# Kernel tuning notes

Measured on AMD Instinct MI355X. Metric: run time of the kernel, lower is better.

The kernel has to match this reference:

```python
import jax, jax.numpy as jnp
import numpy as np

B, Q, PAST = 2, 1024, 1024
T = Q + PAST
HID, NH, NKV, HD = 4096, 32, 8, 128
MAXPOS = 4096
SCALE = HD ** -0.5


def setup_inputs() -> dict:
    key = jax.random.key(0)
    ks = jax.random.split(key, 8)
    hidden_states = jax.random.normal(ks[0], (B, Q, HID), jnp.float32)
    attention_mask = jnp.ones((B, T), jnp.int32)  # all tokens valid
    position_ids = jnp.broadcast_to(
        jnp.arange(PAST, PAST + Q, dtype=jnp.int64)[None, :], (B, Q))
    # standard RoPE caches: [max_pos, head_dim/2]
    inv = 1.0 / (10000.0 ** (np.arange(0, HD, 2, dtype=np.float64) / HD))
    ang = np.arange(MAXPOS, dtype=np.float64)[:, None] * inv[None, :]
    rope_cos_freqs = jnp.asarray(np.cos(ang), jnp.float32)
    rope_sin_freqs = jnp.asarray(np.sin(ang), jnp.float32)
    past_key = jax.random.normal(ks[1], (B, NKV, PAST, HD), jnp.float32)
    past_value = jax.random.normal(ks[2], (B, NKV, PAST, HD), jnp.float32)
    q_w = jax.random.normal(ks[3], (NH * HD, HID), jnp.float32) * 0.02
    k_w = jax.random.normal(ks[4], (NKV * HD, HID), jnp.float32) * 0.02
    v_w = jax.random.normal(ks[5], (NKV * HD, HID), jnp.float32) * 0.02
    o_w = jax.random.normal(ks[6], (HID, NH * HD), jnp.float32) * 0.02
    return {"hidden_states": hidden_states, "attention_mask": attention_mask,
            "position_ids": position_ids, "rope_cos_freqs": rope_cos_freqs,
            "rope_sin_freqs": rope_sin_freqs, "past_key": past_key,
            "past_value": past_value, "q_w": q_w, "k_w": k_w, "v_w": v_w,
            "o_w": o_w}


def _rope(x, cos, sin):
    # x: [B,S,n_heads,HD]; cos/sin: [B,S,HD/2]; non-interleaved (half split)
    d2 = x.shape[-1] // 2
    x1, x2 = x[..., :d2], x[..., d2:]
    c, s = cos[:, :, None, :], sin[:, :, None, :]
    return jnp.concatenate([x1 * c - x2 * s, x2 * c + x1 * s], axis=-1)


def reference(hidden_states, attention_mask, position_ids, rope_cos_freqs,
              rope_sin_freqs, past_key, past_value, q_w, k_w, v_w, o_w):
    b, q_len, _ = hidden_states.shape
    q = jnp.einsum('bsh,oh->bso', hidden_states, q_w).reshape(b, q_len, NH, HD)
    k = jnp.einsum('bsh,oh->bso', hidden_states, k_w).reshape(b, q_len, NKV, HD)
    v = jnp.einsum('bsh,oh->bso', hidden_states, v_w).reshape(b, q_len, NKV, HD)

    cos = rope_cos_freqs[position_ids]  # [B,Q,HD/2]
    sin = rope_sin_freqs[position_ids]
    q = _rope(q, cos, sin)
    k = _rope(k, cos, sin)

    # append to KV cache -> [B,NKV,T,HD]
    present_key = jnp.concatenate([past_key, k.transpose(0, 2, 1, 3)], axis=2)
    present_value = jnp.concatenate([past_value, v.transpose(0, 2, 1, 3)], axis=2)

    # additive causal + padding mask built from cumsum of attention_mask
    all_idx = jnp.cumsum(attention_mask, axis=-1)            # [B,T]
    full = (all_idx[:, -q_len:, None] >= all_idx[:, None, :]) \
        & attention_mask[:, None, :].astype(bool)            # [B,Q,T]
    bias = jnp.where(full, 0.0, -10000.0)[:, None, :, :]     # [B,1,Q,T]

    group = NH // NKV
    k_rep = jnp.repeat(present_key, group, axis=1)           # [B,NH,T,HD]
    v_rep = jnp.repeat(present_value, group, axis=1)

    scores = jnp.einsum('bqhd,bhkd->bhqk', q, k_rep) * SCALE + bias
    probs = jax.nn.softmax(scores, axis=-1)
    ctx = jnp.einsum('bhqk,bhkd->bqhd', probs, v_rep).reshape(b, q_len, NH * HD)
    attn_out = jnp.einsum('bso,ho->bsh', ctx, o_w)
    return attn_out, present_key, present_value
```

## Files before the change

kernel.cpp:

```cpp
#include <hip/hip_runtime.h>
#include <hip/hip_bf16.h>
#include <stdint.h>

typedef __bf16 bf16_t;
typedef bf16_t bf16x8 __attribute__((ext_vector_type(8)));
typedef bf16_t bf16x4 __attribute__((ext_vector_type(4)));
typedef float f32x4 __attribute__((ext_vector_type(4)));

#define B_ 2
#define Q_ 1024
#define PAST_ 1024
#define T_ 2048
#define HID_ 4096
#define NH_ 32
#define NKV_ 8
#define HD_ 128
#define SCALE_ 0.08838834764831845f

__device__ __forceinline__ void async_cp16(const bf16_t* g, bf16_t* l) {
  __builtin_amdgcn_global_load_lds((__attribute__((address_space(1))) void*)g,
                                   (__attribute__((address_space(3))) void*)l, 16, 0, 0);
}

__global__ void cvt_f32_bf16(const float* __restrict__ src, bf16_t* __restrict__ dst, size_t n) {
  size_t i = ((size_t)blockIdx.x * blockDim.x + threadIdx.x) * 8;
  if (i >= n) return;
  float4 a = *(const float4*)(src + i);
  float4 b = *(const float4*)(src + i + 4);
  bf16x8 o;
  o[0] = (bf16_t)a.x; o[1] = (bf16_t)a.y; o[2] = (bf16_t)a.z; o[3] = (bf16_t)a.w;
  o[4] = (bf16_t)b.x; o[5] = (bf16_t)b.y; o[6] = (bf16_t)b.z; o[7] = (bf16_t)b.w;
  *(bf16x8*)(dst + i) = o;
}

__global__ void copy_past(const float* __restrict__ pk, const float* __restrict__ pv,
                          float* __restrict__ oK, float* __restrict__ oV,
                          bf16_t* __restrict__ Kall) {
  size_t i = ((size_t)blockIdx.x * 256 + threadIdx.x) * 4;
  if (i >= (size_t)B_ * NKV_ * PAST_ * HD_) return;
  int d = (int)(i & 127);
  size_t r = i >> 7;
  int t = (int)(r & 1023); r >>= 10;
  int g = (int)(r & 7); int b = (int)(r >> 3);
  size_t dst = (((size_t)b * NKV_ + g) * T_ + t) * HD_ + d;
  float4 k4 = *(const float4*)(pk + i);
  float4 v4 = *(const float4*)(pv + i);
  *(float4*)(oK + dst) = k4;
  *(float4*)(oV + dst) = v4;
  bf16x4 kb; kb[0] = (bf16_t)k4.x; kb[1] = (bf16_t)k4.y; kb[2] = (bf16_t)k4.z; kb[3] = (bf16_t)k4.w;
  *(bf16x4*)(Kall + dst) = kb;
}

__global__ void build_vt(const float* __restrict__ past_v, const float* __restrict__ QKV,
                         bf16_t* __restrict__ Vt) {
  __shared__ bf16_t tile[64][136];
  const int tid = threadIdx.x;
  const int t0 = blockIdx.x * 64, g = blockIdx.y, b = blockIdx.z;
#pragma unroll
  for (int k = 0; k < 8; ++k) {
    int idx = k * 256 + tid;
    int t = idx >> 5, dc = (idx & 31) * 4;
    int tt = t0 + t;
    const float* src = (tt < PAST_)
        ? past_v + ((((size_t)b * NKV_ + g) * PAST_ + tt) * HD_ + dc)
        : QKV + (((size_t)b * Q_ + (tt - PAST_)) * 6144 + 5120 + g * HD_ + dc);
    float4 v4 = *(const float4*)src;
    tile[t][dc] = (bf16_t)v4.x; tile[t][dc + 1] = (bf16_t)v4.y;
    tile[t][dc + 2] = (bf16_t)v4.z; tile[t][dc + 3] = (bf16_t)v4.w;
  }
  __syncthreads();
#pragma unroll
  for (int k = 0; k < 4; ++k) {
    int idx = k * 256 + tid;
    int d = idx >> 3, c = idx & 7;
    bf16x8 o;
#pragma unroll
    for (int j = 0; j < 8; ++j) o[j] = tile[c * 8 + j][d];
    *(bf16x8*)(Vt + ((((size_t)b * NKV_ + g) * HD_ + d) * T_) + t0 + c * 8) = o;
  }
}

__global__ __launch_bounds__(256)
void gemm_bt(const bf16_t* __restrict__ A, const bf16_t* __restrict__ W,
             float* __restrict__ C, int M, int N, int K) {
  __shared__ bf16_t lA[128 * 64];
  __shared__ bf16_t lB[128 * 64];
  const int tid = threadIdx.x;
  const int wave = tid >> 6, lane = tid & 63;
  const int quad = lane >> 4, l15 = lane & 15;
  const int bm = blockIdx.y * 128, bn = blockIdx.x * 128;
  const int wm = (wave >> 1) * 64, wn = (wave & 1) * 64;
  f32x4 acc[4][4] = {};
  for (int k0 = 0; k0 < K; k0 += 64) {
    __syncthreads();
#pragma unroll
    for (int t = 0; t < 4; ++t) {
      int cb = t * 256 + wave * 64;
      int c = cb + lane;
      int row = c >> 3, sc = (c & 7) ^ (row & 7);
      async_cp16(A + (size_t)(bm + row) * K + k0 + sc * 8, lA + (size_t)cb * 8);
      async_cp16(W + (size_t)(bn + row) * K + k0 + sc * 8, lB + (size_t)cb * 8);
    }
    __syncthreads();
#pragma unroll
    for (int ks = 0; ks < 2; ++ks) {
      bf16x8 af[4], bfr[4];
      int lchunk = ks * 4 + quad;
      int pc = (lchunk ^ (l15 & 7)) * 8;
#pragma unroll
      for (int i = 0; i < 4; ++i) af[i] = *(const bf16x8*)(lA + (wm + i * 16 + l15) * 64 + pc);
#pragma unroll
      for (int j = 0; j < 4; ++j) bfr[j] = *(const bf16x8*)(lB + (wn + j * 16 + l15) * 64 + pc);
#pragma unroll
      for (int i = 0; i < 4; ++i)
#pragma unroll
        for (int j = 0; j < 4; ++j)
          acc[i][j] = __builtin_amdgcn_mfma_f32_16x16x32_bf16(af[i], bfr[j], acc[i][j], 0, 0, 0);
    }
  }
#pragma unroll
  for (int i = 0; i < 4; ++i) {
    int row0 = bm + wm + i * 16 + quad * 4;
#pragma unroll
    for (int j = 0; j < 4; ++j) {
      int col = bn + wn + j * 16 + l15;
#pragma unroll
      for (int r = 0; r < 4; ++r)
        C[(size_t)(row0 + r) * N + col] = acc[i][j][r];
    }
  }
}

__global__ void rope_scatter(const float* __restrict__ QKV, const float* __restrict__ cosf,
                             const float* __restrict__ sinf, const int* __restrict__ pos_ids,
                             bf16_t* __restrict__ Qr, bf16_t* __restrict__ Kall,
                             float* __restrict__ outK, float* __restrict__ outV) {
  int m = blockIdx.x;
  int b = m >> 10, s = m & 1023;
  int pos = pos_ids[(size_t)b * Q_ + s];
  const float* row = QKV + (size_t)m * 6144;
  int tid = threadIdx.x;
  for (int p = tid; p < NH_ * 64; p += 256) {
    int h = p >> 6, d = p & 63;
    float x1 = row[h * 128 + d], x2 = row[h * 128 + d + 64];
    float c = cosf[pos * 64 + d], sn = sinf[pos * 64 + d];
    size_t qb = (((size_t)b * NH_ + h) * Q_ + s) * HD_;
    Qr[qb + d] = (bf16_t)(x1 * c - x2 * sn);
    Qr[qb + d + 64] = (bf16_t)(x2 * c + x1 * sn);
  }
  for (int p = tid; p < NKV_ * 64; p += 256) {
    int g = p >> 6, d = p & 63;
    float x1 = row[4096 + g * 128 + d], x2 = row[4096 + g * 128 + d + 64];
    float c = cosf[pos * 64 + d], sn = sinf[pos * 64 + d];
    float o1 = x1 * c - x2 * sn, o2 = x2 * c + x1 * sn;
    size_t kbi = (((size_t)b * NKV_ + g) * T_ + PAST_ + s) * HD_;
    Kall[kbi + d] = (bf16_t)o1; Kall[kbi + d + 64] = (bf16_t)o2;
    outK[kbi + d] = o1; outK[kbi + d + 64] = o2;
  }
  for (int e = tid; e < NKV_ * HD_; e += 256) {
    int g = e >> 7, d = e & 127;
    float v = row[5120 + g * 128 + d];
    outV[(((size_t)b * NKV_ + g) * T_ + PAST_ + s) * HD_ + d] = v;
  }
}

__global__ __launch_bounds__(256, 4)
void attn_fwd(const bf16_t* __restrict__ Qr, const bf16_t* __restrict__ Kall,
              const bf16_t* __restrict__ Vt, bf16_t* __restrict__ Ctx) {
  __shared__ bf16_t lK[64 * 128];
  __shared__ bf16_t lV[128 * 64];
  __shared__ bf16_t lP[4 * 16 * 64];
  const int tid = threadIdx.x;
  const int wave = tid >> 6, lane = tid & 63;
  const int quad = lane >> 4, l15 = lane & 15;
  const int i = blockIdx.x;
  const int xcd = i & 7;
  const int j = i >> 3;
  const int pairsel = j & 1;
  const int idx = j >> 1;
  const int h_in = idx & 3;
  const int qt = 15 - (idx >> 2);
  const int b = pairsel, kv = xcd;
  const int h = kv * 4 + h_in;
  const int qbase = qt * 64;
  const int wq = qbase + wave * 16;
  const size_t kvbase = ((size_t)b * NKV_ + kv) * T_ * HD_;
  const size_t vtbase = ((size_t)b * NKV_ + kv) * HD_ * T_;
  bf16x8 qf[4];
  {
    const bf16_t* qg = Qr + ((((size_t)b * NH_ + h) * Q_) + wq + l15) * HD_ + quad * 8;
#pragma unroll
    for (int kk = 0; kk < 4; ++kk) qf[kk] = *(const bf16x8*)(qg + kk * 32);
  }
  f32x4 ctx[8] = {};
  float Mr[4], Lr[4];
#pragma unroll
  for (int r = 0; r < 4; ++r) { Mr[r] = -3.0e30f; Lr[r] = 0.0f; }
  bf16_t* lPw = lP + wave * 16 * 64;
  const int kend = PAST_ + qbase + 64;
  const int wlimit = PAST_ + wq + 15;
  for (int kb = 0; kb < kend; kb += 64) {
    __syncthreads();
#pragma unroll
    for (int t = 0; t < 4; ++t) {
      int cb = t * 256 + wave * 64;
      int c = cb + lane;
      int row = c >> 4, sc = (c & 15) ^ (row & 15);
      async_cp16(Kall + kvbase + (size_t)(kb + row) * HD_ + sc * 8, lK + (size_t)cb * 8);
    }
#pragma unroll
    for (int t = 0; t < 4; ++t) {
      int cb = t * 256 + wave * 64;
      int c = cb + lane;
      int d = c >> 3, sc = (c & 7) ^ (d & 7);
      async_cp16(Vt + vtbase + (size_t)d * T_ + kb + sc * 8, lV + (size_t)cb * 8);
    }
    __syncthreads();
    if (kb <= wlimit) {
      f32x4 sacc[4];
#pragma unroll
      for (int nc = 0; nc < 4; ++nc) sacc[nc] = (f32x4){0.f, 0.f, 0.f, 0.f};
#pragma unroll
      for (int nc = 0; nc < 4; ++nc)
#pragma unroll
        for (int kk = 0; kk < 4; ++kk) {
          bf16x8 bk = *(const bf16x8*)(lK + (nc * 16 + l15) * 128 + (((kk * 4 + quad) ^ l15) << 3));
          sacc[nc] = __builtin_amdgcn_mfma_f32_16x16x32_bf16(qf[kk], bk, sacc[nc], 0, 0, 0);
        }
      bool fullvis = (kb + 63 <= PAST_ + wq);
#pragma unroll
      for (int nc = 0; nc < 4; ++nc) {
        int tkey = kb + nc * 16 + l15;
#pragma unroll
        for (int r = 0; r < 4; ++r) {
          float val = sacc[nc][r] * SCALE_;
          if (!fullvis && tkey > PAST_ + wq + quad * 4 + r) val -= 10000.0f;
          sacc[nc][r] = val;
        }
      }
      float alpha[4], rs[4] = {};
#pragma unroll
      for (int r = 0; r < 4; ++r) {
        float tm = fmaxf(fmaxf(sacc[0][r], sacc[1][r]), fmaxf(sacc[2][r], sacc[3][r]));
#pragma unroll
        for (int mmk = 1; mmk < 16; mmk <<= 1) tm = fmaxf(tm, __shfl_xor(tm, mmk, 64));
        float nm = fmaxf(Mr[r], tm);
        alpha[r] = __expf(Mr[r] - nm);
        Mr[r] = nm;
      }
#pragma unroll
      for (int nc = 0; nc < 4; ++nc)
#pragma unroll
        for (int r = 0; r < 4; ++r) {
          float p = __expf(sacc[nc][r] - Mr[r]);
          rs[r] += p;
          int rho = quad * 4 + r;
          int cslot = ((nc * 2 + (l15 >> 3)) ^ (rho & 7));
          lPw[rho * 64 + cslot * 8 + (l15 & 7)] = (bf16_t)p;
        }
#pragma unroll
      for (int r = 0; r < 4; ++r) {
        float s = rs[r];
#pragma unroll
        for (int mmk = 1; mmk < 16; mmk <<= 1) s += __shfl_xor(s, mmk, 64);
        Lr[r] = Lr[r] * alpha[r] + s;
      }
#pragma unroll
      for (int nc2 = 0; nc2 < 8; ++nc2)
#pragma unroll
        for (int r = 0; r < 4; ++r) ctx[nc2][r] *= alpha[r];
      asm volatile("s_waitcnt lgkmcnt(0)" ::: "memory");
#pragma unroll
      for (int kk2 = 0; kk2 < 2; ++kk2) {
        bf16x8 ap = *(const bf16x8*)(lPw + l15 * 64 + (((kk2 * 4 + quad) ^ (l15 & 7)) << 3));
#pragma unroll
        for (int nc2 = 0; nc2 < 8; ++nc2) {
          bf16x8 bv = *(const bf16x8*)(lV + (nc2 * 16 + l15) * 64 + (((kk2 * 4 + quad) ^ (l15 & 7)) << 3));
          ctx[nc2] = __builtin_amdgcn_mfma_f32_16x16x32_bf16(ap, bv, ctx[nc2], 0, 0, 0);
        }
      }
    }
  }
  float inv[4];
#pragma unroll
  for (int r = 0; r < 4; ++r) inv[r] = 1.0f / Lr[r];
#pragma unroll
  for (int nc2 = 0; nc2 < 8; ++nc2)
#pragma unroll
    for (int r = 0; r < 4; ++r) {
      size_t row = (size_t)b * Q_ + wq + quad * 4 + r;
      Ctx[row * (NH_ * HD_) + h * HD_ + nc2 * 16 + l15] = (bf16_t)(ctx[nc2][r] * inv[r]);
    }
}

extern "C" void kernel_launch(void* const* d_in, const int* in_sizes, int n_in,
                              void* d_out, int out_size, void* d_ws, size_t ws_size,
                              hipStream_t stream) {
  const float* hidden = (const float*)d_in[0];
  const int* pos = (const int*)d_in[2];
  const float* cosf = (const float*)d_in[3];
  const float* sinf = (const float*)d_in[4];
  const float* past_k = (const float*)d_in[5];
  const float* past_v = (const float*)d_in[6];
  const float* q_w = (const float*)d_in[7];
  const float* k_w = (const float*)d_in[8];
  const float* v_w = (const float*)d_in[9];
  const float* o_w = (const float*)d_in[10];

  float* attn_out = (float*)d_out;
  float* outK = attn_out + (size_t)B_ * Q_ * HID_;
  float* outV = outK + (size_t)B_ * NKV_ * T_ * HD_;

  if (ws_size < 150994944) return;
  char* ws = (char*)d_ws;
  bf16_t* Wqkv = (bf16_t*)(ws);
  bf16_t* Xb   = (bf16_t*)(ws + 50331648);
  float*  QKV  = (float*)(ws + 67108864);
  bf16_t* Qr   = (bf16_t*)(ws + 117440512);
  bf16_t* Kall = (bf16_t*)(ws + 134217728);
  bf16_t* Vt   = (bf16_t*)(ws + 142606336);
  bf16_t* Wo   = (bf16_t*)(ws + 67108864);
  bf16_t* Ctx  = (bf16_t*)(ws + 50331648);

  cvt_f32_bf16<<<4096, 256, 0, stream>>>(hidden, Xb, 8388608);
  cvt_f32_bf16<<<8192, 256, 0, stream>>>(q_w, Wqkv, 16777216);
  cvt_f32_bf16<<<2048, 256, 0, stream>>>(k_w, Wqkv + 16777216, 4194304);
  cvt_f32_bf16<<<2048, 256, 0, stream>>>(v_w, Wqkv + 20971520, 4194304);
  copy_past<<<2048, 256, 0, stream>>>(past_k, past_v, outK, outV, Kall);
  gemm_bt<<<dim3(48, 16), 256, 0, stream>>>(Xb, Wqkv, QKV, 2048, 6144, 4096);
  rope_scatter<<<2048, 256, 0, stream>>>(QKV, cosf, sinf, pos, Qr, Kall, outK, outV);
  build_vt<<<dim3(32, 8, 2), 256, 0, stream>>>(past_v, QKV, Vt);
  cvt_f32_bf16<<<8192, 256, 0, stream>>>(o_w, Wo, 16777216);
  attn_fwd<<<1024, 256, 0, stream>>>(Qr, Kall, Vt, Ctx);
  gemm_bt<<<dim3(32, 16), 256, 0, stream>>>(Ctx, Wo, attn_out, 2048, 4096, 4096);
}
```

Before: 613.2 us.

## Replace 128x128 GEMM with 256x256 double-buffered, 8-wave pipelined GEMM kernel

```diff
diff --git a/kernel.cpp b/kernel.cpp
--- a/kernel.cpp
+++ b/kernel.cpp
@@ -80,53 +80,141 @@
   }
 }
 
-__global__ __launch_bounds__(256)
-void gemm_bt(const bf16_t* __restrict__ A, const bf16_t* __restrict__ W,
+__device__ __forceinline__ void stage_tile(const bf16_t* __restrict__ G, int ldg,
+                                           bf16_t* __restrict__ L, int tid) {
+#pragma unroll
+  for (int t = 0; t < 4; ++t) {
+    int c = t * 512 + tid;
+    int row = c >> 3, sc = (c & 7) ^ (row & 7);
+    int cb = t * 512 + (tid & 448);
+    async_cp16(G + (size_t)row * ldg + sc * 8, L + (size_t)cb * 8);
+  }
+}
+
+__global__ __launch_bounds__(512, 2)
+void gemm256(const bf16_t* __restrict__ A, const bf16_t* __restrict__ W,
              float* __restrict__ C, int M, int N, int K) {
-  __shared__ bf16_t lA[128 * 64];
-  __shared__ bf16_t lB[128 * 64];
+  __shared__ bf16_t sm[2][2][16384];
   const int tid = threadIdx.x;
-  const int wave = tid >> 6, lane = tid & 63;
+  const int lane = tid & 63;
   const int quad = lane >> 4, l15 = lane & 15;
-  const int bm = blockIdx.y * 128, bn = blockIdx.x * 128;
-  const int wm = (wave >> 1) * 64, wn = (wave & 1) * 64;
-  f32x4 acc[4][4] = {};
-  for (int k0 = 0; k0 < K; k0 += 64) {
-    __syncthreads();
-#pragma unroll
-    for (int t = 0; t < 4; ++t) {
-      int cb = t * 256 + wave * 64;
-      int c = cb + lane;
-      int row = c >> 3, sc = (c & 7) ^ (row & 7);
-      async_cp16(A + (size_t)(bm + row) * K + k0 + sc * 8, lA + (size_t)cb * 8);
-      async_cp16(W + (size_t)(bn + row) * K + k0 + sc * 8, lB + (size_t)cb * 8);
-    }
-    __syncthreads();
-#pragma unroll
-    for (int ks = 0; ks < 2; ++ks) {
-      bf16x8 af[4], bfr[4];
-      int lchunk = ks * 4 + quad;
-      int pc = (lchunk ^ (l15 & 7)) * 8;
-#pragma unroll
-      for (int i = 0; i < 4; ++i) af[i] = *(const bf16x8*)(lA + (wm + i * 16 + l15) * 64 + pc);
-#pragma unroll
-      for (int j = 0; j < 4; ++j) bfr[j] = *(const bf16x8*)(lB + (wn + j * 16 + l15) * 64 + pc);
-#pragma unroll
-      for (int i = 0; i < 4; ++i)
-#pragma unroll
-        for (int j = 0; j < 4; ++j)
-          acc[i][j] = __builtin_amdgcn_mfma_f32_16x16x32_bf16(af[i], bfr[j], acc[i][j], 0, 0, 0);
-    }
-  }
-#pragma unroll
-  for (int i = 0; i < 4; ++i) {
-    int row0 = bm + wm + i * 16 + quad * 4;
-#pragma unroll
-    for (int j = 0; j < 4; ++j) {
-      int col = bn + wn + j * 16 + l15;
+  const int wave = tid >> 6;
+  const int wm = wave >> 2, wn = wave & 3;
+  const int bm = blockIdx.y * 256, bn = blockIdx.x * 256;
+  const int NT = K >> 6;
+
+  const bf16_t* Ag = A + (size_t)bm * K;
+  const bf16_t* Wg = W + (size_t)bn * K;
+
+  f32x4 acc[8][4] = {};
+
+  stage_tile(Ag, K, &sm[0][0][0], tid);
+  stage_tile(Wg, K, &sm[0][1][0], tid);
+  stage_tile(Ag + 64, K, &sm[1][0][0], tid);
+  stage_tile(Wg + 64, K, &sm[1][1][0], tid);
+  asm volatile("s_waitcnt vmcnt(8)" ::: "memory");
+  __builtin_amdgcn_s_barrier();
+
+  const int arow = wm * 128 + l15;
+  const int brow = wn * 64 + l15;
+  const int pq = l15 & 7;
+
+  for (int t = 0; t < NT; ++t) {
+    const bf16_t* lA = &sm[t & 1][0][0];
+    const bf16_t* lB = &sm[t & 1][1][0];
+    const int k2 = (t + 2) << 6;
+    bf16x8 af[4][2], bf01[2][2], bf23[2][2];
+
+#pragma unroll
+    for (int m = 0; m < 4; ++m)
+#pragma unroll
+      for (int kk = 0; kk < 2; ++kk)
+        af[m][kk] = *(const bf16x8*)(lA + (arow + m * 16) * 64 + ((((kk << 2) + quad) ^ pq) << 3));
+#pragma unroll
+    for (int n = 0; n < 2; ++n)
+#pragma unroll
+      for (int kk = 0; kk < 2; ++kk)
+        bf01[n][kk] = *(const bf16x8*)(lB + (brow + n * 16) * 64 + ((((kk << 2) + quad) ^ pq) << 3));
+    __builtin_amdgcn_s_barrier();
+    asm volatile("s_waitcnt lgkmcnt(0)" ::: "memory");
+    __builtin_amdgcn_sched_barrier(0);
+    __builtin_amdgcn_s_setprio(1);
+#pragma unroll
+    for (int m = 0; m < 4; ++m)
+#pragma unroll
+      for (int n = 0; n < 2; ++n)
+#pragma unroll
+        for (int kk = 0; kk < 2; ++kk)
+          acc[m][n] = __builtin_amdgcn_mfma_f32_16x16x32_bf16(af[m][kk], bf01[n][kk], acc[m][n], 0, 0, 0);
+    __builtin_amdgcn_s_setprio(0);
+    __builtin_amdgcn_s_barrier();
+
+#pragma unroll
+    for (int n = 0; n < 2; ++n)
+#pragma unroll
+      for (int kk = 0; kk < 2; ++kk)
+        bf23[n][kk] = *(const bf16x8*)(lB + (brow + (n + 2) * 16) * 64 + ((((kk << 2) + quad) ^ pq) << 3));
+    __builtin_amdgcn_s_barrier();
+    asm volatile("s_waitcnt lgkmcnt(0)" ::: "memory");
+    __builtin_amdgcn_sched_barrier(0);
+    __builtin_amdgcn_s_setprio(1);
+#pragma unroll
+    for (int m = 0; m < 4; ++m)
+#pragma unroll
+      for (int n = 0; n < 2; ++n)
+#pragma unroll
+        for (int kk = 0; kk < 2; ++kk)
+          acc[m][n + 2] = __builtin_amdgcn_mfma_f32_16x16x32_bf16(af[m][kk], bf23[n][kk], acc[m][n + 2], 0, 0, 0);
+    __builtin_amdgcn_s_setprio(0);
+    __builtin_amdgcn_s_barrier();
+
+#pragma unroll
+    for (int m = 0; m < 4; ++m)
+#pragma unroll
+      for (int kk = 0; kk < 2; ++kk)
+        af[m][kk] = *(const bf16x8*)(lA + (arow + (m + 4) * 16) * 64 + ((((kk << 2) + quad) ^ pq) << 3));
+    if (t + 2 < NT) stage_tile(Wg + k2, K, &sm[t & 1][1][0], tid);
+    __builtin_amdgcn_s_barrier();
+    asm volatile("s_waitcnt lgkmcnt(0)" ::: "memory");
+    __builtin_amdgcn_sched_barrier(0);
+    __builtin_amdgcn_s_setprio(1);
+#pragma unroll
+    for (int m = 0; m < 4; ++m)
+#pragma unroll
+      for (int n = 0; n < 2; ++n)
+#pragma unroll
+        for (int kk = 0; kk < 2; ++kk)
+          acc[m + 4][n + 2] = __builtin_amdgcn_mfma_f32_16x16x32_bf16(af[m][kk], bf23[n][kk], acc[m + 4][n + 2], 0, 0, 0);
+    __builtin_amdgcn_s_setprio(0);
+    __builtin_amdgcn_s_barrier();
+
+    if (t + 2 < NT) stage_tile(Ag + k2, K, &sm[t & 1][0][0], tid);
+    __builtin_amdgcn_s_barrier();
+    __builtin_amdgcn_s_setprio(1);
+#pragma unroll
+    for (int m = 0; m < 4; ++m)
+#pragma unroll
+      for (int n = 0; n < 2; ++n)
+#pragma unroll
+        for (int kk = 0; kk < 2; ++kk)
+          acc[m + 4][n] = __builtin_amdgcn_mfma_f32_16x16x32_bf16(af[m][kk], bf01[n][kk], acc[m + 4][n], 0, 0, 0);
+    __builtin_amdgcn_s_setprio(0);
+    if (t + 2 < NT)
+      asm volatile("s_waitcnt vmcnt(8)" ::: "memory");
+    else if (t + 2 == NT)
+      asm volatile("s_waitcnt vmcnt(0)" ::: "memory");
+    __builtin_amdgcn_s_barrier();
+  }
+
+#pragma unroll
+  for (int m = 0; m < 8; ++m) {
+    int row0 = bm + wm * 128 + m * 16 + quad * 4;
+#pragma unroll
+    for (int n = 0; n < 4; ++n) {
+      int col = bn + wn * 64 + n * 16 + l15;
 #pragma unroll
       for (int r = 0; r < 4; ++r)
-        C[(size_t)(row0 + r) * N + col] = acc[i][j][r];
+        C[(size_t)(row0 + r) * N + col] = acc[m][n][r];
     }
   }
 }
@@ -327,10 +415,10 @@
   cvt_f32_bf16<<<2048, 256, 0, stream>>>(k_w, Wqkv + 16777216, 4194304);
   cvt_f32_bf16<<<2048, 256, 0, stream>>>(v_w, Wqkv + 20971520, 4194304);
   copy_past<<<2048, 256, 0, stream>>>(past_k, past_v, outK, outV, Kall);
-  gemm_bt<<<dim3(48, 16), 256, 0, stream>>>(Xb, Wqkv, QKV, 2048, 6144, 4096);
+  gemm256<<<dim3(24, 8), 512, 0, stream>>>(Xb, Wqkv, QKV, 2048, 6144, 4096);
   rope_scatter<<<2048, 256, 0, stream>>>(QKV, cosf, sinf, pos, Qr, Kall, outK, outV);
   build_vt<<<dim3(32, 8, 2), 256, 0, stream>>>(past_v, QKV, Vt);
   cvt_f32_bf16<<<8192, 256, 0, stream>>>(o_w, Wo, 16777216);
   attn_fwd<<<1024, 256, 0, stream>>>(Qr, Kall, Vt, Ctx);
-  gemm_bt<<<dim3(32, 16), 256, 0, stream>>>(Ctx, Wo, attn_out, 2048, 4096, 4096);
-}
+  gemm256<<<dim3(16, 8), 512, 0, stream>>>(Ctx, Wo, attn_out, 2048, 4096, 4096);
+}
```

Result: no change. 624.6 us (+1.9%).
